# Kernel tuning notes

Hardware: AMD Instinct MI355X
Metric: run time of the kernel (lower is better)

The kernel has to match this reference:

```python
import jax, jax.numpy as jnp
import numpy as np
from jax import lax

EPS = 1e-5
BETA = 0.2  # commitment loss weight


def _conv(x, w, b, stride=2, pad=1):
    # torch Conv2d(k=4, s=2, p=1), NCHW / OIHW
    y = lax.conv_general_dilated(x, w, (stride, stride), [(pad, pad), (pad, pad)],
                                 dimension_numbers=('NCHW', 'OIHW', 'NCHW'))
    return y + b[None, :, None, None]


def _convT(x, w, b):
    # torch ConvTranspose2d(k=4, s=2, p=1): dilated conv with flipped kernel,
    # effective pad = k - 1 - p = 2. w is torch layout [in, out, kH, kW].
    wt = jnp.flip(w, (2, 3)).transpose(1, 0, 2, 3)  # -> [out, in, kH, kW]
    y = lax.conv_general_dilated(x, wt, (1, 1), [(2, 2), (2, 2)], lhs_dilation=(2, 2),
                                 dimension_numbers=('NCHW', 'OIHW', 'NCHW'))
    return y + b[None, :, None, None]


def _bn(x, g, b):
    # BatchNorm2d in training mode: per-channel batch statistics (biased var)
    m = x.mean((0, 2, 3), keepdims=True)
    v = x.var((0, 2, 3), keepdims=True)
    xn = (x - m) * lax.rsqrt(v + EPS)
    return g[None, :, None, None] * xn + b[None, :, None, None]


def _forward(x, enc_w1, enc_b1, enc_w2, enc_b2, enc_w3, enc_b3,
             enc_g1, enc_be1, enc_g2, enc_be2, enc_g3, enc_be3,
             codebook,
             dec_w1, dec_b1, dec_w2, dec_b2, dec_w3, dec_b3,
             dec_g1, dec_be1, dec_g2, dec_be2, dec_g3, dec_be3):
    # ---- Encoder: [B,1,256,256] -> [B,32,32,32] ----
    h = jax.nn.relu(_bn(_conv(x, enc_w1, enc_b1), enc_g1, enc_be1))
    h = jax.nn.relu(_bn(_conv(h, enc_w2, enc_b2), enc_g2, enc_be2))
    q_in = jax.nn.relu(_bn(_conv(h, enc_w3, enc_b3), enc_g3, enc_be3))

    B, C, H, W = q_in.shape
    # ---- Quantiser: cdist + argmin + codebook gather ----
    z = q_in.transpose(0, 2, 3, 1).reshape(B, H * W, C)  # [B, HW, C]
    # squared euclidean distance (same argmin as torch.cdist)
    d2 = (jnp.sum(z * z, -1, keepdims=True)
          - 2.0 * jnp.einsum('bnc,kc->bnk', z, codebook)
          + jnp.sum(codebook * codebook, -1))  # [B, HW, K]
    idx = jnp.argmin(d2, axis=-1)  # [B, HW] int
    q_out = codebook[idx].reshape(B, H, W, C).transpose(0, 3, 1, 2)  # [B,C,H,W]

    commitment = jnp.mean((lax.stop_gradient(q_out) - q_in) ** 2)
    codebook_l = jnp.mean((q_out - lax.stop_gradient(q_in)) ** 2)
    quant_loss = codebook_l + BETA * commitment
    # straight-through estimator
    q_st = q_in + lax.stop_gradient(q_out - q_in)
    encoding_indices = idx.reshape(-1, H, W)

    # ---- Decoder: [B,32,32,32] -> [B,1,256,256] ----
    d = jax.nn.relu(_bn(_convT(q_st, dec_w1, dec_b1), dec_g1, dec_be1))
    d = jax.nn.relu(_bn(_convT(d, dec_w2, dec_b2), dec_g2, dec_be2))
    out = _bn(_convT(d, dec_w3, dec_b3), dec_g3, dec_be3)

    recon = jnp.mean((x - out) ** 2)
    total_loss = quant_loss + recon
    return out, total_loss, encoding_indices


def setup_inputs() -> dict:
    key = jax.random.key(0)
    ks = jax.random.split(key, 12)
    rn = lambda k, s, sc=0.05: jax.random.normal(k, s, jnp.float32) * sc
    inp = {
        'x': jax.random.normal(ks[0], (64, 1, 256, 256), jnp.float32),
        'enc_w1': rn(ks[1], (16, 1, 4, 4)),  'enc_b1': jnp.zeros((16,), jnp.float32),
        'enc_w2': rn(ks[2], (16, 16, 4, 4)), 'enc_b2': jnp.zeros((16,), jnp.float32),
        'enc_w3': rn(ks[3], (32, 16, 4, 4)), 'enc_b3': jnp.zeros((32,), jnp.float32),
        'enc_g1': jnp.ones((16,), jnp.float32), 'enc_be1': jnp.zeros((16,), jnp.float32),
        'enc_g2': jnp.ones((16,), jnp.float32), 'enc_be2': jnp.zeros((16,), jnp.float32),
        'enc_g3': jnp.ones((32,), jnp.float32), 'enc_be3': jnp.zeros((32,), jnp.float32),
        'codebook': jax.random.normal(ks[4], (512, 32), jnp.float32),  # nn.Embedding ~ N(0,1)
        'dec_w1': rn(ks[5], (32, 16, 4, 4)), 'dec_b1': jnp.zeros((16,), jnp.float32),  # [in,out,kH,kW]
        'dec_w2': rn(ks[6], (16, 16, 4, 4)), 'dec_b2': jnp.zeros((16,), jnp.float32),
        'dec_w3': rn(ks[7], (16, 1, 4, 4)),  'dec_b3': jnp.zeros((1,), jnp.float32),
        'dec_g1': jnp.ones((16,), jnp.float32), 'dec_be1': jnp.zeros((16,), jnp.float32),
        'dec_g2': jnp.ones((16,), jnp.float32), 'dec_be2': jnp.zeros((16,), jnp.float32),
        'dec_g3': jnp.ones((1,), jnp.float32),  'dec_be3': jnp.zeros((1,), jnp.float32),
    }
    return inp


def reference(x, enc_w1, enc_b1, enc_w2, enc_b2, enc_w3, enc_b3,
              enc_g1, enc_be1, enc_g2, enc_be2, enc_g3, enc_be3,
              codebook,
              dec_w1, dec_b1, dec_w2, dec_b2, dec_w3, dec_b3,
              dec_g1, dec_be1, dec_g2, dec_be2, dec_g3, dec_be3):
    return _forward(x, enc_w1, enc_b1, enc_w2, enc_b2, enc_w3, enc_b3,
                    enc_g1, enc_be1, enc_g2, enc_be2, enc_g3, enc_be3,
                    codebook,
                    dec_w1, dec_b1, dec_w2, dec_b2, dec_w3, dec_b3,
                    dec_g1, dec_be1, dec_g2, dec_be2, dec_g3, dec_be3)
```

## Files before the change

kernel.cpp:

```cpp
#include <hip/hip_runtime.h>

#define BLK 256


template<int CO>
__device__ __forceinline__ void block_stats(const float* acc, float* partOut) {
  __shared__ float red[2][CO][4];
  const int lane = threadIdx.x & 63;
  const int wv   = threadIdx.x >> 6;
#pragma unroll
  for (int co = 0; co < CO; ++co) {
    float s = acc[co];
    float q = s * s;
#pragma unroll
    for (int off = 32; off > 0; off >>= 1) {
      s += __shfl_down(s, off, 64);
      q += __shfl_down(q, off, 64);
    }
    if (lane == 0) { red[0][co][wv] = s; red[1][co][wv] = q; }
  }
  __syncthreads();
  if (threadIdx.x < CO) {
    const int co = threadIdx.x;
    float s = red[0][co][0] + red[0][co][1] + red[0][co][2] + red[0][co][3];
    float q = red[1][co][0] + red[1][co][1] + red[1][co][2] + red[1][co][3];
    partOut[co * 2]     = s;
    partOut[co * 2 + 1] = q;
  }
}

__device__ __forceinline__ void block_stats2(float s, float q, float* partOut) {
  __shared__ float red2[2][4];
  const int lane = threadIdx.x & 63;
  const int wv   = threadIdx.x >> 6;
#pragma unroll
  for (int off = 32; off > 0; off >>= 1) {
    s += __shfl_down(s, off, 64);
    q += __shfl_down(q, off, 64);
  }
  if (lane == 0) { red2[0][wv] = s; red2[1][wv] = q; }
  __syncthreads();
  if (threadIdx.x == 0) {
    partOut[0] = red2[0][0] + red2[0][1] + red2[0][2] + red2[0][3];
    partOut[1] = red2[1][0] + red2[1][1] + red2[1][2] + red2[1][3];
  }
}


template<int CI, int CO, int HIN, int WIN, bool BN_IN>
__global__ __launch_bounds__(BLK) void conv_k(
    const float* __restrict__ in, const float* __restrict__ w,
    const float* __restrict__ bias,
    const float* __restrict__ scIn, const float* __restrict__ shIn,
    float* __restrict__ out, float* __restrict__ part)
{
  constexpr int HOUT = HIN / 2, WOUT = WIN / 2;
  __shared__ float wl[CO * CI * 16];
  for (int i = threadIdx.x; i < CO * CI * 16; i += BLK) wl[i] = w[i];
  float sc[CI], sh[CI];
  if constexpr (BN_IN) {
#pragma unroll
    for (int ci = 0; ci < CI; ++ci) { sc[ci] = scIn[ci]; sh[ci] = shIn[ci]; }
  }
  __syncthreads();

  const int idx = blockIdx.x * BLK + threadIdx.x;
  const int ow  = idx % WOUT;
  const int oh  = (idx / WOUT) % HOUT;
  const int b   = idx / (WOUT * HOUT);

  float acc[CO];
#pragma unroll
  for (int co = 0; co < CO; ++co) acc[co] = bias[co];

  const float* inb = in + (size_t)b * CI * HIN * WIN;

#pragma unroll
  for (int kh = 0; kh < 4; ++kh) {
    const int ih = oh * 2 - 1 + kh;
    if ((unsigned)ih < (unsigned)HIN) {
#pragma unroll
      for (int kw = 0; kw < 4; ++kw) {
        const int iw = ow * 2 - 1 + kw;
        if ((unsigned)iw < (unsigned)WIN) {
#pragma unroll 2
          for (int ci = 0; ci < CI; ++ci) {
            float v = inb[(ci * HIN + ih) * WIN + iw];
            if constexpr (BN_IN) v = fmaxf(fmaf(sc[ci], v, sh[ci]), 0.f);
#pragma unroll
            for (int co = 0; co < CO; ++co)
              acc[co] = fmaf(v, wl[((co * CI + ci) * 4 + kh) * 4 + kw], acc[co]);
          }
        }
      }
    }
  }

#pragma unroll
  for (int co = 0; co < CO; ++co)
    out[((size_t)(b * CO + co) * HOUT + oh) * WOUT + ow] = acc[co];

  block_stats<CO>(acc, part + (size_t)blockIdx.x * CO * 2);
}


template<int CI, int CO, int HIN, int WIN, bool BN_IN>
__global__ __launch_bounds__(BLK) void convT_k(
    const float* __restrict__ in, const float* __restrict__ w,
    const float* __restrict__ bias,
    const float* __restrict__ scIn, const float* __restrict__ shIn,
    float* __restrict__ out, float* __restrict__ part)
{
  constexpr int HOUT = HIN * 2, WOUT = WIN * 2;
  __shared__ float wl[CI * CO * 16];
  for (int i = threadIdx.x; i < CI * CO * 16; i += BLK) wl[i] = w[i];
  float sc[CI], sh[CI];
  if constexpr (BN_IN) {
#pragma unroll
    for (int ci = 0; ci < CI; ++ci) { sc[ci] = scIn[ci]; sh[ci] = shIn[ci]; }
  }
  __syncthreads();

  const int idx = blockIdx.x * BLK + threadIdx.x;
  const int ow  = idx % WOUT;
  const int oh  = (idx / WOUT) % HOUT;
  const int b   = idx / (WOUT * HOUT);

  float acc[CO];
#pragma unroll
  for (int co = 0; co < CO; ++co) acc[co] = bias[co];

  const float* inb = in + (size_t)b * CI * HIN * WIN;
  const int kh0 = 1 - (oh & 1);
  const int kw0 = 1 - (ow & 1);

#pragma unroll
  for (int th = 0; th < 2; ++th) {
    const int kh  = kh0 + 2 * th;
    const int ihh = oh + 1 - kh;
    const int ih  = ihh >> 1;
    if (ihh >= 0 && ih < HIN) {
#pragma unroll
      for (int tw = 0; tw < 2; ++tw) {
        const int kw  = kw0 + 2 * tw;
        const int iww = ow + 1 - kw;
        const int iw  = iww >> 1;
        if (iww >= 0 && iw < WIN) {
#pragma unroll 2
          for (int ci = 0; ci < CI; ++ci) {
            float v = inb[(ci * HIN + ih) * WIN + iw];
            if constexpr (BN_IN) v = fmaxf(fmaf(sc[ci], v, sh[ci]), 0.f);
#pragma unroll
            for (int co = 0; co < CO; ++co)
              acc[co] = fmaf(v, wl[((ci * CO + co) * 4 + kh) * 4 + kw], acc[co]);
          }
        }
      }
    }
  }

#pragma unroll
  for (int co = 0; co < CO; ++co)
    out[((size_t)(b * CO + co) * HOUT + oh) * WOUT + ow] = acc[co];

  block_stats<CO>(acc, part + (size_t)blockIdx.x * CO * 2);
}


__global__ __launch_bounds__(BLK) void convT3q_k(
    const float* __restrict__ in, const float* __restrict__ w,
    const float* __restrict__ bias,
    const float* __restrict__ scIn, const float* __restrict__ shIn,
    float* __restrict__ out, float* __restrict__ part)
{
  __shared__ float wl[256];
  wl[threadIdx.x] = w[threadIdx.x];
  float sc[16], sh[16];
#pragma unroll
  for (int ci = 0; ci < 16; ++ci) { sc[ci] = scIn[ci]; sh[ci] = shIn[ci]; }
  const float b0 = bias[0];
  __syncthreads();

  const int idx = blockIdx.x * BLK + threadIdx.x;
  const int tx = idx & 63;
  const int ty = (idx >> 6) & 63;
  const int b  = idx >> 12;
  const int i0 = ty * 2, j0 = tx * 2;

  constexpr int TAP[4][4] = {{1,1,3,0},{0,2,2,1},{1,2,3,1},{0,3,2,2}};

  float acc[4][4];
#pragma unroll
  for (int r = 0; r < 4; ++r)
#pragma unroll
    for (int c = 0; c < 4; ++c) acc[r][c] = b0;

  const float* inb = in + (size_t)b * 16 * 16384;

#pragma unroll 4
  for (int ci = 0; ci < 16; ++ci) {
    const float sci = sc[ci], shi = sh[ci];
    const float* base = inb + ci * 16384;
    float v[4][4];
#pragma unroll
    for (int pr = 0; pr < 4; ++pr) {
      const int ih = i0 - 1 + pr;
      const bool okr = (unsigned)ih < 128u;
#pragma unroll
      for (int pc = 0; pc < 4; ++pc) {
        const int iw = j0 - 1 + pc;
        float val = 0.f;
        if (okr && (unsigned)iw < 128u)
          val = fmaxf(fmaf(sci, base[ih * 128 + iw], shi), 0.f);
        v[pr][pc] = val;
      }
    }
    const float4 w0 = *(const float4*)&wl[ci * 16 + 0];
    const float4 w1 = *(const float4*)&wl[ci * 16 + 4];
    const float4 w2 = *(const float4*)&wl[ci * 16 + 8];
    const float4 w3 = *(const float4*)&wl[ci * 16 + 12];
    const float wg[16] = {w0.x,w0.y,w0.z,w0.w, w1.x,w1.y,w1.z,w1.w,
                          w2.x,w2.y,w2.z,w2.w, w3.x,w3.y,w3.z,w3.w};
#pragma unroll
    for (int r = 0; r < 4; ++r) {
      const int k1r = TAP[r][0], p1r = TAP[r][1], k2r = TAP[r][2], p2r = TAP[r][3];
#pragma unroll
      for (int c = 0; c < 4; ++c) {
        const int k1c = TAP[c][0], p1c = TAP[c][1], k2c = TAP[c][2], p2c = TAP[c][3];
        float a = acc[r][c];
        a = fmaf(v[p1r][p1c], wg[k1r * 4 + k1c], a);
        a = fmaf(v[p1r][p2c], wg[k1r * 4 + k2c], a);
        a = fmaf(v[p2r][p1c], wg[k2r * 4 + k1c], a);
        a = fmaf(v[p2r][p2c], wg[k2r * 4 + k2c], a);
        acc[r][c] = a;
      }
    }
  }

  float* ob = out + (size_t)b * 65536;
#pragma unroll
  for (int r = 0; r < 4; ++r) {
    float4 o;
    o.x = acc[r][0]; o.y = acc[r][1]; o.z = acc[r][2]; o.w = acc[r][3];
    *(float4*)&ob[(ty * 4 + r) * 256 + tx * 4] = o;
  }

  float s = 0.f, q = 0.f;
#pragma unroll
  for (int r = 0; r < 4; ++r)
#pragma unroll
    for (int c = 0; c < 4; ++c) { s += acc[r][c]; q = fmaf(acc[r][c], acc[r][c], q); }
  block_stats2(s, q, part + (size_t)blockIdx.x * 2);
}


template<int C>
__global__ __launch_bounds__(BLK) void stats_k(
    const float* __restrict__ part, int nB, double N,
    const float* __restrict__ g, const float* __restrict__ be,
    float* __restrict__ sc, float* __restrict__ sh)
{
  const int c = blockIdx.x;
  double s0 = 0.0, s1 = 0.0;
  for (int i = threadIdx.x; i < nB; i += BLK) {
    s0 += (double)part[(size_t)i * C * 2 + c * 2];
    s1 += (double)part[(size_t)i * C * 2 + c * 2 + 1];
  }
  __shared__ double lds[8];
  const int lane = threadIdx.x & 63, wv = threadIdx.x >> 6;
#pragma unroll
  for (int off = 32; off > 0; off >>= 1) {
    s0 += __shfl_down(s0, off, 64);
    s1 += __shfl_down(s1, off, 64);
  }
  if (lane == 0) { lds[wv * 2] = s0; lds[wv * 2 + 1] = s1; }
  __syncthreads();
  if (threadIdx.x == 0) {
    s0 = lds[0] + lds[2] + lds[4] + lds[6];
    s1 = lds[1] + lds[3] + lds[5] + lds[7];
    const double mean = s0 / N;
    const double var  = s1 / N - mean * mean;
    const double inv  = 1.0 / sqrt(var + 1e-5);
    sc[c] = (float)((double)g[c] * inv);
    sh[c] = (float)((double)be[c] - mean * (double)g[c] * inv);
  }
}


__global__ __launch_bounds__(BLK) void cbn_k(const float* __restrict__ cbg,
                                             float* __restrict__ cbn)
{
  const int k = blockIdx.x * BLK + threadIdx.x;
  float s = 0.f;
#pragma unroll
  for (int c = 0; c < 32; ++c) {
    const float x = cbg[k * 32 + c];
    s = fmaf(x, x, s);
  }
  cbn[k] = s;
}

__global__ __launch_bounds__(BLK) void quantp_k(
    const float* __restrict__ y3, const float* __restrict__ cbg,
    const float* __restrict__ cbnG,
    const float* __restrict__ sc, const float* __restrict__ sh,
    float* __restrict__ bd, int* __restrict__ bki)
{
  __shared__ float cb[64 * 32];
  __shared__ float cbnl[64];
  const int pblk  = blockIdx.x & 63;
  const int chunk = blockIdx.x >> 6;
  for (int i = threadIdx.x; i < 2048; i += BLK) cb[i] = cbg[chunk * 2048 + i];
  if (threadIdx.x < 64) cbnl[threadIdx.x] = cbnG[chunk * 64 + threadIdx.x];
  __syncthreads();

  const int pos0 = pblk * 1024 + threadIdx.x;

  float z[4][32];
#pragma unroll
  for (int c = 0; c < 32; ++c) {
    const float s_ = sc[c], h_ = sh[c];
#pragma unroll
    for (int j = 0; j < 4; ++j) {
      const int pos = pos0 + j * 256;
      const int bb = pos >> 10, pp = pos & 1023;
      z[j][c] = fmaxf(fmaf(s_, y3[((size_t)(bb * 32 + c)) * 1024 + pp], h_), 0.f);
    }
  }

  float best[4] = {3.402823466e38f, 3.402823466e38f, 3.402823466e38f, 3.402823466e38f};
  int   bk[4]   = {0, 0, 0, 0};

  for (int k = 0; k < 64; ++k) {
    const float4* row = (const float4*)&cb[k * 32];
    float d[4] = {0.f, 0.f, 0.f, 0.f};
#pragma unroll
    for (int c4 = 0; c4 < 8; ++c4) {
      const float4 cc = row[c4];
#pragma unroll
      for (int j = 0; j < 4; ++j) {
        d[j] = fmaf(z[j][c4 * 4 + 0], cc.x, d[j]);
        d[j] = fmaf(z[j][c4 * 4 + 1], cc.y, d[j]);
        d[j] = fmaf(z[j][c4 * 4 + 2], cc.z, d[j]);
        d[j] = fmaf(z[j][c4 * 4 + 3], cc.w, d[j]);
      }
    }
    const float cl = cbnl[k];
    const int kk = chunk * 64 + k;
#pragma unroll
    for (int j = 0; j < 4; ++j) {
      const float dd = cl - 2.f * d[j];
      if (dd < best[j]) { best[j] = dd; bk[j] = kk; }
    }
  }

#pragma unroll
  for (int j = 0; j < 4; ++j) {
    const int pos = pos0 + j * 256;
    bd[chunk * 65536 + pos]  = best[j];
    bki[chunk * 65536 + pos] = bk[j];
  }
}

__global__ __launch_bounds__(BLK) void quantm_k(
    const float* __restrict__ y3, const float* __restrict__ cbg,
    const float* __restrict__ sc, const float* __restrict__ sh,
    const float* __restrict__ bd, const int* __restrict__ bki,
    float* __restrict__ qout, float* __restrict__ idx_out,
    float* __restrict__ pq)
{
  const int pos = blockIdx.x * BLK + threadIdx.x;
  float best = 3.402823466e38f;
  int bk = 0;
#pragma unroll
  for (int s = 0; s < 8; ++s) {
    const float d = bd[s * 65536 + pos];
    const int   k = bki[s * 65536 + pos];
    if (d < best) { best = d; bk = k; }
  }

  const int b = pos >> 10, p = pos & 1023;
  const float4* qrow = (const float4*)(cbg + (size_t)bk * 32);
  float msd = 0.f;
#pragma unroll
  for (int c4 = 0; c4 < 8; ++c4) {
    const float4 q4 = qrow[c4];
    const float qv[4] = {q4.x, q4.y, q4.z, q4.w};
#pragma unroll
    for (int u = 0; u < 4; ++u) {
      const int c = c4 * 4 + u;
      const float v  = y3[((size_t)(b * 32 + c)) * 1024 + p];
      const float zz = fmaxf(fmaf(sc[c], v, sh[c]), 0.f);
      const float qq = qv[u];
      qout[((size_t)(b * 32 + c)) * 1024 + p] = zz + (qq - zz);
      const float df = qq - zz;
      msd = fmaf(df, df, msd);
    }
  }
  idx_out[pos] = (float)bk;
  block_stats2(msd, 0.f, pq + (size_t)blockIdx.x * 2);
}


__global__ __launch_bounds__(BLK) void final4_k(
    const float* __restrict__ y6, const float* __restrict__ x,
    const float* __restrict__ sc, const float* __restrict__ sh,
    float* __restrict__ out, float* __restrict__ pr)
{
  const size_t i = ((size_t)blockIdx.x * BLK + threadIdx.x) * 4;
  const float s0 = sc[0], h0 = sh[0];
  const float4 yv = *(const float4*)(y6 + i);
  const float4 xv = *(const float4*)(x + i);
  float4 ov;
  ov.x = fmaf(s0, yv.x, h0);
  ov.y = fmaf(s0, yv.y, h0);
  ov.z = fmaf(s0, yv.z, h0);
  ov.w = fmaf(s0, yv.w, h0);
  *(float4*)(out + i) = ov;
  const float d0 = xv.x - ov.x, d1 = xv.y - ov.y, d2 = xv.z - ov.z, d3 = xv.w - ov.w;
  float s = d0 * d0;
  s = fmaf(d1, d1, s);
  s = fmaf(d2, d2, s);
  s = fmaf(d3, d3, s);
  block_stats2(s, 0.f, pr + (size_t)blockIdx.x * 2);
}


__global__ __launch_bounds__(BLK) void loss_k(
    const float* __restrict__ pq, const float* __restrict__ pr,
    float* __restrict__ lossOut)
{
  double s = 0.0, r = 0.0;
  for (int i = threadIdx.x; i < 256; i += BLK)  s += (double)pq[i * 2];
  for (int i = threadIdx.x; i < 4096; i += BLK) r += (double)pr[i * 2];
  __shared__ double lds[8];
  const int lane = threadIdx.x & 63, wv = threadIdx.x >> 6;
#pragma unroll
  for (int off = 32; off > 0; off >>= 1) {
    s += __shfl_down(s, off, 64);
    r += __shfl_down(r, off, 64);
  }
  if (lane == 0) { lds[wv * 2] = s; lds[wv * 2 + 1] = r; }
  __syncthreads();
  if (threadIdx.x == 0) {
    s = lds[0] + lds[2] + lds[4] + lds[6];
    r = lds[1] + lds[3] + lds[5] + lds[7];
    lossOut[0] = (float)(1.2 * (s / 2097152.0) + r / 4194304.0);
  }
}


extern "C" void kernel_launch(void* const* d_in, const int* in_sizes, int n_in,
                              void* d_out, int out_size, void* d_ws, size_t ws_size,
                              hipStream_t stream) {
  const float* x    = (const float*)d_in[0];
  const float* ew1  = (const float*)d_in[1];
  const float* eb1  = (const float*)d_in[2];
  const float* ew2  = (const float*)d_in[3];
  const float* eb2  = (const float*)d_in[4];
  const float* ew3  = (const float*)d_in[5];
  const float* eb3  = (const float*)d_in[6];
  const float* eg1  = (const float*)d_in[7];
  const float* ebe1 = (const float*)d_in[8];
  const float* eg2  = (const float*)d_in[9];
  const float* ebe2 = (const float*)d_in[10];
  const float* eg3  = (const float*)d_in[11];
  const float* ebe3 = (const float*)d_in[12];
  const float* cbk  = (const float*)d_in[13];
  const float* dw1  = (const float*)d_in[14];
  const float* db1  = (const float*)d_in[15];
  const float* dw2  = (const float*)d_in[16];
  const float* db2  = (const float*)d_in[17];
  const float* dw3  = (const float*)d_in[18];
  const float* db3  = (const float*)d_in[19];
  const float* dg1  = (const float*)d_in[20];
  const float* dbe1 = (const float*)d_in[21];
  const float* dg2  = (const float*)d_in[22];
  const float* dbe2 = (const float*)d_in[23];
  const float* dg3  = (const float*)d_in[24];
  const float* dbe3 = (const float*)d_in[25];

  float* ws = (float*)d_ws;
  float* outp = (float*)d_out;

  float* SC = ws;
  float* SH = ws + 192;
  float* P1 = ws + 1024;
  float* P2 = ws + 132096;
  float* P3 = ws + 164864;
  float* P4 = ws + 181248;
  float* P5 = ws + 214016;
  float* P6 = ws + 345088;
  float* Pq = ws + 377856;
  float* Pr = ws + 378368;
  float* CBN = ws + 411648;

  float* y1 = ws + 524288;
  float* y2 = y1 + 16777216;
  float* y3 = y2 + 4194304;
  float* qo = y3 + 2097152;
  float* y6 = qo + 2097152;
  float* y4 = y2;
  float* y5 = y1;
  float* bd  = y2;
  int*   bki = (int*)(y2 + 524288);

  float* sc1 = SC + 0,  *sh1 = SH + 0;
  float* sc2 = SC + 32, *sh2 = SH + 32;
  float* sc3 = SC + 64, *sh3 = SH + 64;
  float* sc4 = SC + 96, *sh4 = SH + 96;
  float* sc5 = SC + 128,*sh5 = SH + 128;
  float* sc6 = SC + 160,*sh6 = SH + 160;

  cbn_k<<<2, BLK, 0, stream>>>(cbk, CBN);

  conv_k<1, 16, 256, 256, false><<<4096, BLK, 0, stream>>>(x,  ew1, eb1, nullptr, nullptr, y1, P1);
  stats_k<16><<<16, BLK, 0, stream>>>(P1, 4096, 1048576.0, eg1, ebe1, sc1, sh1);
  conv_k<16, 16, 128, 128, true><<<1024, BLK, 0, stream>>>(y1, ew2, eb2, sc1, sh1, y2, P2);
  stats_k<16><<<16, BLK, 0, stream>>>(P2, 1024, 262144.0, eg2, ebe2, sc2, sh2);
  conv_k<16, 32, 64, 64, true><<<256, BLK, 0, stream>>>(y2, ew3, eb3, sc2, sh2, y3, P3);
  stats_k<32><<<32, BLK, 0, stream>>>(P3, 256, 65536.0, eg3, ebe3, sc3, sh3);

  quantp_k<<<512, BLK, 0, stream>>>(y3, cbk, CBN, sc3, sh3, bd, bki);
  quantm_k<<<256, BLK, 0, stream>>>(y3, cbk, sc3, sh3, bd, bki, qo, outp + 4194305, Pq);

  convT_k<32, 16, 32, 32, false><<<1024, BLK, 0, stream>>>(qo, dw1, db1, nullptr, nullptr, y4, P4);
  stats_k<16><<<16, BLK, 0, stream>>>(P4, 1024, 262144.0, dg1, dbe1, sc4, sh4);
  convT_k<16, 16, 64, 64, true><<<4096, BLK, 0, stream>>>(y4, dw2, db2, sc4, sh4, y5, P5);
  stats_k<16><<<16, BLK, 0, stream>>>(P5, 4096, 1048576.0, dg2, dbe2, sc5, sh5);
  convT3q_k<<<1024, BLK, 0, stream>>>(y5, dw3, db3, sc5, sh5, y6, P6);
  stats_k<1><<<1, BLK, 0, stream>>>(P6, 1024, 4194304.0, dg3, dbe3, sc6, sh6);

  final4_k<<<4096, BLK, 0, stream>>>(y6, x, sc6, sh6, outp, Pr);
  loss_k<<<1, BLK, 0, stream>>>(Pq, Pr, outp + 4194304);
}
```

Measured before the change: 674.1 us.

## Register-tile encoder conv2 and decoder convT2 over output patches and channel groups

Replaces the generic per-pixel conv and transposed-conv kernels for the 16->16 middle layers with register-blocked versions. For conv2, each thread computes a 2x2 output patch for 8 output channels. For convT2, each thread computes a 4x4 output patch for 4 channels, using a sub-pixel tap mapping. Input patches are loaded once per channel and reused across overlapping kernel taps, weights are read from shared memory as float4 in a reordered layout, and outputs are stored with vector stores. The aim is fewer redundant input loads and normalisations per FMA, in exchange for higher register pressure and fewer blocks.

```diff
diff --git a/kernel.cpp b/kernel.cpp
--- a/kernel.cpp
+++ b/kernel.cpp
@@ -101,6 +101,128 @@
     out[((size_t)(b * CO + co) * HOUT + oh) * WOUT + ow] = acc[co];
 
   block_stats<CO>(acc, part + (size_t)blockIdx.x * CO * 2);
+}
+
+
+__global__ __launch_bounds__(BLK) void conv2r_k(
+    const float* __restrict__ in, const float* __restrict__ w,
+    const float* __restrict__ bias,
+    const float* __restrict__ scIn, const float* __restrict__ shIn,
+    float* __restrict__ out, float* __restrict__ part)
+{
+  __shared__ float wr[4096];
+  __shared__ float red[4][2][8][2];
+  for (int i = threadIdx.x; i < 4096; i += BLK) {
+    const int co = i & 15, kw = (i >> 4) & 3, kh = (i >> 6) & 3, ci = i >> 8;
+    wr[i] = w[((co * 16 + ci) * 4 + kh) * 4 + kw];
+  }
+  float sc[16], sh[16];
+#pragma unroll
+  for (int ci = 0; ci < 16; ++ci) { sc[ci] = scIn[ci]; sh[ci] = shIn[ci]; }
+  __syncthreads();
+
+  const int T  = blockIdx.x * BLK + threadIdx.x;
+  const int cg = T & 1;
+  const int tf = T >> 1;
+  const int tx = tf & 31;
+  const int ty = (tf >> 5) & 31;
+  const int b  = tf >> 10;
+
+  float acc[2][2][8];
+  {
+    const float4 ba = *(const float4*)(bias + cg * 8);
+    const float4 bb = *(const float4*)(bias + cg * 8 + 4);
+    const float bi[8] = {ba.x, ba.y, ba.z, ba.w, bb.x, bb.y, bb.z, bb.w};
+#pragma unroll
+    for (int dy = 0; dy < 2; ++dy)
+#pragma unroll
+      for (int dx = 0; dx < 2; ++dx)
+#pragma unroll
+        for (int j = 0; j < 8; ++j) acc[dy][dx][j] = bi[j];
+  }
+
+  const float* inb = in + (size_t)b * 16 * 16384;
+
+#pragma unroll 2
+  for (int ci = 0; ci < 16; ++ci) {
+    const float sci = sc[ci], shi = sh[ci];
+    const float* base = inb + ci * 16384;
+    float v[6][6];
+#pragma unroll
+    for (int pr = 0; pr < 6; ++pr) {
+      const int ih = 4 * ty - 1 + pr;
+      const bool okr = (unsigned)ih < 128u;
+#pragma unroll
+      for (int pc = 0; pc < 6; ++pc) {
+        const int iw = 4 * tx - 1 + pc;
+        float val = 0.f;
+        if (okr && (unsigned)iw < 128u)
+          val = fmaxf(fmaf(sci, base[ih * 128 + iw], shi), 0.f);
+        v[pr][pc] = val;
+      }
+    }
+#pragma unroll
+    for (int kh = 0; kh < 4; ++kh) {
+#pragma unroll
+      for (int kw = 0; kw < 4; ++kw) {
+        const int wb = ((ci * 4 + kh) * 4 + kw) * 16 + cg * 8;
+        const float4 wa = *(const float4*)&wr[wb];
+        const float4 wc = *(const float4*)&wr[wb + 4];
+        const float wg[8] = {wa.x, wa.y, wa.z, wa.w, wc.x, wc.y, wc.z, wc.w};
+#pragma unroll
+        for (int dy = 0; dy < 2; ++dy)
+#pragma unroll
+          for (int dx = 0; dx < 2; ++dx) {
+            const float pv = v[2 * dy + kh][2 * dx + kw];
+#pragma unroll
+            for (int j = 0; j < 8; ++j)
+              acc[dy][dx][j] = fmaf(pv, wg[j], acc[dy][dx][j]);
+          }
+      }
+    }
+  }
+
+#pragma unroll
+  for (int j = 0; j < 8; ++j)
+#pragma unroll
+    for (int dy = 0; dy < 2; ++dy) {
+      float2 o; o.x = acc[dy][0][j]; o.y = acc[dy][1][j];
+      *(float2*)&out[((size_t)(b * 16 + cg * 8 + j) * 64 + 2 * ty + dy) * 64 + 2 * tx] = o;
+    }
+
+  {
+    float s[8], q[8];
+#pragma unroll
+    for (int j = 0; j < 8; ++j) {
+      float a = acc[0][0][j] + acc[0][1][j] + acc[1][0][j] + acc[1][1][j];
+      float qq = acc[0][0][j] * acc[0][0][j];
+      qq = fmaf(acc[0][1][j], acc[0][1][j], qq);
+      qq = fmaf(acc[1][0][j], acc[1][0][j], qq);
+      qq = fmaf(acc[1][1][j], acc[1][1][j], qq);
+      s[j] = a; q[j] = qq;
+    }
+    const int lane = threadIdx.x & 63, wv = threadIdx.x >> 6;
+#pragma unroll
+    for (int off = 32; off >= 2; off >>= 1)
+#pragma unroll
+      for (int j = 0; j < 8; ++j) {
+        s[j] += __shfl_down(s[j], off, 64);
+        q[j] += __shfl_down(q[j], off, 64);
+      }
+    if (lane < 2) {
+#pragma unroll
+      for (int j = 0; j < 8; ++j) { red[wv][lane][j][0] = s[j]; red[wv][lane][j][1] = q[j]; }
+    }
+    __syncthreads();
+    if (threadIdx.x < 16) {
+      const int g = threadIdx.x >> 3, j = threadIdx.x & 7;
+      float ss = 0.f, qq = 0.f;
+#pragma unroll
+      for (int wvi = 0; wvi < 4; ++wvi) { ss += red[wvi][g][j][0]; qq += red[wvi][g][j][1]; }
+      part[(size_t)blockIdx.x * 32 + (g * 8 + j) * 2]     = ss;
+      part[(size_t)blockIdx.x * 32 + (g * 8 + j) * 2 + 1] = qq;
+    }
+  }
 }
 
 
@@ -164,6 +286,132 @@
     out[((size_t)(b * CO + co) * HOUT + oh) * WOUT + ow] = acc[co];
 
   block_stats<CO>(acc, part + (size_t)blockIdx.x * CO * 2);
+}
+
+
+__global__ __launch_bounds__(BLK) void convT2r_k(
+    const float* __restrict__ in, const float* __restrict__ w,
+    const float* __restrict__ bias,
+    const float* __restrict__ scIn, const float* __restrict__ shIn,
+    float* __restrict__ out, float* __restrict__ part)
+{
+  __shared__ float wr[4096];
+  __shared__ float red[4][4][4][2];
+  for (int i = threadIdx.x; i < 4096; i += BLK) {
+    const int co = i & 15, kw = (i >> 4) & 3, kh = (i >> 6) & 3, ci = i >> 8;
+    wr[i] = w[((ci * 16 + co) * 4 + kh) * 4 + kw];
+  }
+  float sc[16], sh[16];
+#pragma unroll
+  for (int ci = 0; ci < 16; ++ci) { sc[ci] = scIn[ci]; sh[ci] = shIn[ci]; }
+  __syncthreads();
+
+  const int T  = blockIdx.x * BLK + threadIdx.x;
+  const int cg = T & 3;
+  const int tf = T >> 2;
+  const int tx = tf & 31;
+  const int ty = (tf >> 5) & 31;
+  const int b  = tf >> 10;
+
+  constexpr int RKr[4][2] = {{1,3},{0,2},{1,3},{0,2}};
+  constexpr int RKp[4][2] = {{2,3},{1,2},{1,2},{0,1}};
+
+  float acc[4][4][4];
+  {
+    const float4 b4 = *(const float4*)(bias + cg * 4);
+    const float bi[4] = {b4.x, b4.y, b4.z, b4.w};
+#pragma unroll
+    for (int r = 0; r < 4; ++r)
+#pragma unroll
+      for (int c = 0; c < 4; ++c)
+#pragma unroll
+        for (int j = 0; j < 4; ++j) acc[r][c][j] = bi[j];
+  }
+
+  const float* inb = in + (size_t)b * 16 * 4096;
+
+#pragma unroll 2
+  for (int ci = 0; ci < 16; ++ci) {
+    const float sci = sc[ci], shi = sh[ci];
+    const float* base = inb + ci * 4096;
+    float v[4][4];
+#pragma unroll
+    for (int pr = 0; pr < 4; ++pr) {
+      const int ih = 2 * ty - 1 + pr;
+      const bool okr = (unsigned)ih < 64u;
+#pragma unroll
+      for (int pc = 0; pc < 4; ++pc) {
+        const int iw = 2 * tx - 1 + pc;
+        float val = 0.f;
+        if (okr && (unsigned)iw < 64u)
+          val = fmaxf(fmaf(sci, base[ih * 64 + iw], shi), 0.f);
+        v[pr][pc] = val;
+      }
+    }
+#pragma unroll
+    for (int kh = 0; kh < 4; ++kh) {
+#pragma unroll
+      for (int kw = 0; kw < 4; ++kw) {
+        const float4 w4 = *(const float4*)&wr[((ci * 4 + kh) * 4 + kw) * 16 + cg * 4];
+#pragma unroll
+        for (int i2 = 0; i2 < 2; ++i2) {
+          const int r = RKr[kh][i2], pr_ = RKp[kh][i2];
+#pragma unroll
+          for (int j2 = 0; j2 < 2; ++j2) {
+            const int c = RKr[kw][j2], pc_ = RKp[kw][j2];
+            const float pv = v[pr_][pc_];
+            acc[r][c][0] = fmaf(pv, w4.x, acc[r][c][0]);
+            acc[r][c][1] = fmaf(pv, w4.y, acc[r][c][1]);
+            acc[r][c][2] = fmaf(pv, w4.z, acc[r][c][2]);
+            acc[r][c][3] = fmaf(pv, w4.w, acc[r][c][3]);
+          }
+        }
+      }
+    }
+  }
+
+#pragma unroll
+  for (int j = 0; j < 4; ++j)
+#pragma unroll
+    for (int r = 0; r < 4; ++r) {
+      float4 o;
+      o.x = acc[r][0][j]; o.y = acc[r][1][j]; o.z = acc[r][2][j]; o.w = acc[r][3][j];
+      *(float4*)&out[((size_t)(b * 16 + cg * 4 + j) * 128 + 4 * ty + r) * 128 + 4 * tx] = o;
+    }
+
+  {
+    float s[4], q[4];
+#pragma unroll
+    for (int j = 0; j < 4; ++j) {
+      float a = 0.f, qq = 0.f;
+#pragma unroll
+      for (int r = 0; r < 4; ++r)
+#pragma unroll
+        for (int c = 0; c < 4; ++c) { a += acc[r][c][j]; qq = fmaf(acc[r][c][j], acc[r][c][j], qq); }
+      s[j] = a; q[j] = qq;
+    }
+    const int lane = threadIdx.x & 63, wv = threadIdx.x >> 6;
+#pragma unroll
+    for (int off = 32; off >= 4; off >>= 1)
+#pragma unroll
+      for (int j = 0; j < 4; ++j) {
+        s[j] += __shfl_down(s[j], off, 64);
+        q[j] += __shfl_down(q[j], off, 64);
+      }
+    if (lane < 4) {
+#pragma unroll
+      for (int j = 0; j < 4; ++j) { red[wv][lane][j][0] = s[j]; red[wv][lane][j][1] = q[j]; }
+    }
+    __syncthreads();
+    if (threadIdx.x < 16) {
+      const int g = threadIdx.x >> 2, j = threadIdx.x & 3;
+      float ss = 0.f, qq = 0.f;
+#pragma unroll
+      for (int wvi = 0; wvi < 4; ++wvi) { ss += red[wvi][g][j][0]; qq += red[wvi][g][j][1]; }
+      part[(size_t)blockIdx.x * 32 + (g * 4 + j) * 2]     = ss;
+      part[(size_t)blockIdx.x * 32 + (g * 4 + j) * 2 + 1] = qq;
+    }
+  }
 }
 
 
@@ -516,8 +764,8 @@
 
   conv_k<1, 16, 256, 256, false><<<4096, BLK, 0, stream>>>(x,  ew1, eb1, nullptr, nullptr, y1, P1);
   stats_k<16><<<16, BLK, 0, stream>>>(P1, 4096, 1048576.0, eg1, ebe1, sc1, sh1);
-  conv_k<16, 16, 128, 128, true><<<1024, BLK, 0, stream>>>(y1, ew2, eb2, sc1, sh1, y2, P2);
-  stats_k<16><<<16, BLK, 0, stream>>>(P2, 1024, 262144.0, eg2, ebe2, sc2, sh2);
+  conv2r_k<<<512, BLK, 0, stream>>>(y1, ew2, eb2, sc1, sh1, y2, P2);
+  stats_k<16><<<16, BLK, 0, stream>>>(P2, 512, 262144.0, eg2, ebe2, sc2, sh2);
   conv_k<16, 32, 64, 64, true><<<256, BLK, 0, stream>>>(y2, ew3, eb3, sc2, sh2, y3, P3);
   stats_k<32><<<32, BLK, 0, stream>>>(P3, 256, 65536.0, eg3, ebe3, sc3, sh3);
 
@@ -526,8 +774,8 @@
 
   convT_k<32, 16, 32, 32, false><<<1024, BLK, 0, stream>>>(qo, dw1, db1, nullptr, nullptr, y4, P4);
   stats_k<16><<<16, BLK, 0, stream>>>(P4, 1024, 262144.0, dg1, dbe1, sc4, sh4);
-  convT_k<16, 16, 64, 64, true><<<4096, BLK, 0, stream>>>(y4, dw2, db2, sc4, sh4, y5, P5);
-  stats_k<16><<<16, BLK, 0, stream>>>(P5, 4096, 1048576.0, dg2, dbe2, sc5, sh5);
+  convT2r_k<<<1024, BLK, 0, stream>>>(y4, dw2, db2, sc4, sh4, y5, P5);
+  stats_k<16><<<16, BLK, 0, stream>>>(P5, 1024, 1048576.0, dg2, dbe2, sc5, sh5);
   convT3q_k<<<1024, BLK, 0, stream>>>(y5, dw3, db3, sc5, sh5, y6, P6);
   stats_k<1><<<1, BLK, 0, stream>>>(P6, 1024, 4194304.0, dg3, dbe3, sc6, sh6);
 
```

Result: slower. 716.7 us (+6.3%).

## Pre-transpose conv weights to co-contiguous layout and read via scalar loads

Applied to the files above, without the earlier changes.

Adds small kernels that reorder encoder conv and decoder convT weights into [ci][kh][kw][co] layout in workspace. The conv kernels then read weights directly from global memory, contiguous in co and uniform across threads, instead of staging them into LDS with a __syncthreads. The aim is to drop the per-block LDS fill and barrier and allow wide uniform (scalar-cache) loads. In exchange it adds five tiny launches per call, and the weight reads now depend on the constant cache rather than LDS.

```diff
diff --git a/kernel.cpp b/kernel.cpp
--- a/kernel.cpp
+++ b/kernel.cpp
@@ -47,22 +47,44 @@
 }
 
 
+__global__ __launch_bounds__(BLK) void twc_k(const float* __restrict__ w,
+                                             float* __restrict__ wt,
+                                             int CI, int CO) {
+  const int total = CI * CO * 16;
+  for (int i = threadIdx.x; i < total; i += BLK) {
+    const int co = i % CO;
+    const int rest = i / CO;
+    const int kw = rest & 3, kh = (rest >> 2) & 3, ci = rest >> 4;
+    wt[i] = w[(co * CI + ci) * 16 + kh * 4 + kw];
+  }
+}
+
+__global__ __launch_bounds__(BLK) void twt_k(const float* __restrict__ w,
+                                             float* __restrict__ wt,
+                                             int CI, int CO) {
+  const int total = CI * CO * 16;
+  for (int i = threadIdx.x; i < total; i += BLK) {
+    const int co = i % CO;
+    const int rest = i / CO;
+    const int kw = rest & 3, kh = (rest >> 2) & 3, ci = rest >> 4;
+    wt[i] = w[(ci * CO + co) * 16 + kh * 4 + kw];
+  }
+}
+
+
 template<int CI, int CO, int HIN, int WIN, bool BN_IN>
-__global__ __launch_bounds__(BLK) void conv_k(
-    const float* __restrict__ in, const float* __restrict__ w,
+__global__ __launch_bounds__(BLK) void conv_s(
+    const float* __restrict__ in, const float* __restrict__ wt,
     const float* __restrict__ bias,
     const float* __restrict__ scIn, const float* __restrict__ shIn,
     float* __restrict__ out, float* __restrict__ part)
 {
   constexpr int HOUT = HIN / 2, WOUT = WIN / 2;
-  __shared__ float wl[CO * CI * 16];
-  for (int i = threadIdx.x; i < CO * CI * 16; i += BLK) wl[i] = w[i];
   float sc[CI], sh[CI];
   if constexpr (BN_IN) {
 #pragma unroll
     for (int ci = 0; ci < CI; ++ci) { sc[ci] = scIn[ci]; sh[ci] = shIn[ci]; }
   }
-  __syncthreads();
 
   const int idx = blockIdx.x * BLK + threadIdx.x;
   const int ow  = idx % WOUT;
@@ -87,9 +109,10 @@
           for (int ci = 0; ci < CI; ++ci) {
             float v = inb[(ci * HIN + ih) * WIN + iw];
             if constexpr (BN_IN) v = fmaxf(fmaf(sc[ci], v, sh[ci]), 0.f);
+            const float* wrow = wt + ((ci * 4 + kh) * 4 + kw) * CO;
 #pragma unroll
             for (int co = 0; co < CO; ++co)
-              acc[co] = fmaf(v, wl[((co * CI + ci) * 4 + kh) * 4 + kw], acc[co]);
+              acc[co] = fmaf(v, wrow[co], acc[co]);
           }
         }
       }
@@ -105,21 +128,18 @@
 
 
 template<int CI, int CO, int HIN, int WIN, bool BN_IN>
-__global__ __launch_bounds__(BLK) void convT_k(
-    const float* __restrict__ in, const float* __restrict__ w,
+__global__ __launch_bounds__(BLK) void convT_s(
+    const float* __restrict__ in, const float* __restrict__ wt,
     const float* __restrict__ bias,
     const float* __restrict__ scIn, const float* __restrict__ shIn,
     float* __restrict__ out, float* __restrict__ part)
 {
   constexpr int HOUT = HIN * 2, WOUT = WIN * 2;
-  __shared__ float wl[CI * CO * 16];
-  for (int i = threadIdx.x; i < CI * CO * 16; i += BLK) wl[i] = w[i];
   float sc[CI], sh[CI];
   if constexpr (BN_IN) {
 #pragma unroll
     for (int ci = 0; ci < CI; ++ci) { sc[ci] = scIn[ci]; sh[ci] = shIn[ci]; }
   }
-  __syncthreads();
 
   const int idx = blockIdx.x * BLK + threadIdx.x;
   const int ow  = idx % WOUT;
@@ -150,9 +170,10 @@
           for (int ci = 0; ci < CI; ++ci) {
             float v = inb[(ci * HIN + ih) * WIN + iw];
             if constexpr (BN_IN) v = fmaxf(fmaf(sc[ci], v, sh[ci]), 0.f);
+            const float* wrow = wt + ((ci * 4 + kh) * 4 + kw) * CO;
 #pragma unroll
             for (int co = 0; co < CO; ++co)
-              acc[co] = fmaf(v, wl[((ci * CO + co) * 4 + kh) * 4 + kw], acc[co]);
+              acc[co] = fmaf(v, wrow[co], acc[co]);
           }
         }
       }
@@ -494,6 +515,11 @@
   float* Pq = ws + 377856;
   float* Pr = ws + 378368;
   float* CBN = ws + 411648;
+  float* WT1  = ws + 412160;
+  float* WT2  = WT1 + 256;
+  float* WT3  = WT2 + 4096;
+  float* WTD1 = WT3 + 8192;
+  float* WTD2 = WTD1 + 8192;
 
   float* y1 = ws + 524288;
   float* y2 = y1 + 16777216;
@@ -512,21 +538,26 @@
   float* sc5 = SC + 128,*sh5 = SH + 128;
   float* sc6 = SC + 160,*sh6 = SH + 160;
 
+  twc_k<<<1, BLK, 0, stream>>>(ew1, WT1, 1, 16);
+  twc_k<<<1, BLK, 0, stream>>>(ew2, WT2, 16, 16);
+  twc_k<<<1, BLK, 0, stream>>>(ew3, WT3, 16, 32);
+  twt_k<<<1, BLK, 0, stream>>>(dw1, WTD1, 32, 16);
+  twt_k<<<1, BLK, 0, stream>>>(dw2, WTD2, 16, 16);
   cbn_k<<<2, BLK, 0, stream>>>(cbk, CBN);
 
-  conv_k<1, 16, 256, 256, false><<<4096, BLK, 0, stream>>>(x,  ew1, eb1, nullptr, nullptr, y1, P1);
+  conv_s<1, 16, 256, 256, false><<<4096, BLK, 0, stream>>>(x,  WT1, eb1, nullptr, nullptr, y1, P1);
   stats_k<16><<<16, BLK, 0, stream>>>(P1, 4096, 1048576.0, eg1, ebe1, sc1, sh1);
-  conv_k<16, 16, 128, 128, true><<<1024, BLK, 0, stream>>>(y1, ew2, eb2, sc1, sh1, y2, P2);
+  conv_s<16, 16, 128, 128, true><<<1024, BLK, 0, stream>>>(y1, WT2, eb2, sc1, sh1, y2, P2);
   stats_k<16><<<16, BLK, 0, stream>>>(P2, 1024, 262144.0, eg2, ebe2, sc2, sh2);
-  conv_k<16, 32, 64, 64, true><<<256, BLK, 0, stream>>>(y2, ew3, eb3, sc2, sh2, y3, P3);
+  conv_s<16, 32, 64, 64, true><<<256, BLK, 0, stream>>>(y2, WT3, eb3, sc2, sh2, y3, P3);
   stats_k<32><<<32, BLK, 0, stream>>>(P3, 256, 65536.0, eg3, ebe3, sc3, sh3);
 
   quantp_k<<<512, BLK, 0, stream>>>(y3, cbk, CBN, sc3, sh3, bd, bki);
   quantm_k<<<256, BLK, 0, stream>>>(y3, cbk, sc3, sh3, bd, bki, qo, outp + 4194305, Pq);
 
-  convT_k<32, 16, 32, 32, false><<<1024, BLK, 0, stream>>>(qo, dw1, db1, nullptr, nullptr, y4, P4);
+  convT_s<32, 16, 32, 32, false><<<1024, BLK, 0, stream>>>(qo, WTD1, db1, nullptr, nullptr, y4, P4);
   stats_k<16><<<16, BLK, 0, stream>>>(P4, 1024, 262144.0, dg1, dbe1, sc4, sh4);
-  convT_k<16, 16, 64, 64, true><<<4096, BLK, 0, stream>>>(y4, dw2, db2, sc4, sh4, y5, P5);
+  convT_s<16, 16, 64, 64, true><<<4096, BLK, 0, stream>>>(y4, WTD2, db2, sc4, sh4, y5, P5);
   stats_k<16><<<16, BLK, 0, stream>>>(P5, 4096, 1048576.0, dg2, dbe2, sc5, sh5);
   convT3q_k<<<1024, BLK, 0, stream>>>(y5, dw3, db3, sc5, sh5, y6, P6);
   stats_k<1><<<1, BLK, 0, stream>>>(P6, 1024, 4194304.0, dg3, dbe3, sc6, sh6);
```

After: 674.8 us. About the same (+0.1%).
